# Performance work log

Measured on AMD Instinct MI355X. Metric: run time of the kernel, lower is better.

Reference implementation:

```python
import jax, jax.numpy as jnp
import numpy as np

D_MODEL = 768
N_HEADS = 12
D_K = D_MODEL // N_HEADS
NEG = -1e9


def setup_inputs() -> dict:
    key = jax.random.key(0)
    ks = jax.random.split(key, 10)
    B, S = 2, 2048
    x = jax.random.normal(ks[0], (B, S, D_MODEL), dtype=jnp.float32)
    # causal mask, broadcastable over batch and heads
    mask = jnp.tril(jnp.ones((S, S), dtype=jnp.int32))[None, None]
    scale = 1.0 / np.sqrt(D_MODEL)
    def lin(k):
        return jax.random.normal(k, (D_MODEL, D_MODEL), dtype=jnp.float32) * scale
    return {
        "x": x, "mask": mask,
        "wq": lin(ks[1]), "bq": jnp.zeros((D_MODEL,), jnp.float32),
        "wk": lin(ks[2]), "bk": jnp.zeros((D_MODEL,), jnp.float32),
        "wv": lin(ks[3]), "bv": jnp.zeros((D_MODEL,), jnp.float32),
        "wo": lin(ks[4]), "bo": jnp.zeros((D_MODEL,), jnp.float32),
    }


def reference(x, mask, wq, bq, wk, bk, wv, bv, wo, bo):
    B, S, _ = x.shape
    def split_heads(t):  # [B,S,D] -> [B,H,S,dk]
        return t.reshape(B, S, N_HEADS, D_K).transpose(0, 2, 1, 3)
    q = split_heads(x @ wq + bq)
    k = split_heads(x @ wk + bk)
    v = split_heads(x @ wv + bv)
    scores = jnp.einsum("bhqd,bhkd->bhqk", q, k) / jnp.sqrt(jnp.float32(D_K))
    scores = jnp.where(mask == 0, NEG, scores)
    attn = jax.nn.softmax(scores, axis=-1)
    # dropout is identity in eval mode
    ctx = jnp.einsum("bhqk,bhkd->bhqd", attn, v)
    ctx = ctx.transpose(0, 2, 1, 3).reshape(B, S, D_MODEL)
    return ctx @ wo + bo
```

## Files before the change

### kernel.cpp

```cpp
#include <hip/hip_runtime.h>
#include <hip/hip_bf16.h>
#include <stdint.h>

#define DM   768
#define NH   12
#define DKH  64
#define BB   2
#define SS   2048
#define MT   (BB*SS)
#define NQKV (3*DM)

typedef __attribute__((ext_vector_type(8))) short short8;
typedef __attribute__((ext_vector_type(4))) float f32x4;

__device__ __forceinline__ unsigned short f2bf(float f) {
    union { float f; unsigned u; } v; v.f = f;
    unsigned r = v.u + 0x7fffu + ((v.u >> 16) & 1u);
    return (unsigned short)(r >> 16);
}

__device__ __forceinline__ void gload_lds16(const unsigned short* g, unsigned short* l) {
    __builtin_amdgcn_global_load_lds((const __attribute__((address_space(1))) void*)g,
                                     (__attribute__((address_space(3))) void*)l, 16, 0, 0);
}

__launch_bounds__(256)
__global__ void k_conv(const float* __restrict__ x, unsigned short* __restrict__ xb,
                       const float* __restrict__ wq, const float* __restrict__ wk,
                       const float* __restrict__ wv, const float* __restrict__ wo,
                       unsigned short* __restrict__ wT) {
    __shared__ float tile[32][33];
    const int t = threadIdx.x;
    if (blockIdx.x < 3072) {
        int i = blockIdx.x * 256 + t;
        const float4 v = ((const float4*)x)[i];
        ushort4 o;
        o.x = f2bf(v.x); o.y = f2bf(v.y); o.z = f2bf(v.z); o.w = f2bf(v.w);
        ((ushort4*)xb)[i] = o;
    } else {
        const int cid = blockIdx.x - 3072;
        const int sel = cid / 576;
        const int rem = cid - sel * 576;
        const int kb = rem / 24, nb = rem - (rem / 24) * 24;
        const float* w = (sel == 0) ? wq : (sel == 1) ? wk : (sel == 2) ? wv : wo;
        const int k0 = kb * 32, n0 = nb * 32;
        const int tx = t & 31, ty = t >> 5;
        #pragma unroll
        for (int j = 0; j < 4; j++)
            tile[ty + 8*j][tx] = w[(size_t)(k0 + ty + 8*j) * DM + n0 + tx];
        __syncthreads();
        #pragma unroll
        for (int j = 0; j < 4; j++)
            wT[(size_t)(sel*DM + n0 + ty + 8*j) * DM + k0 + tx] = f2bf(tile[tx][ty + 8*j]);
    }
}

__launch_bounds__(256)
__global__ void k_gemm_qkv(const unsigned short* __restrict__ xb,
                           const unsigned short* __restrict__ wT,
                           const float* __restrict__ bq, const float* __restrict__ bk,
                           const float* __restrict__ bv,
                           unsigned short* __restrict__ Qb,
                           unsigned short* __restrict__ Kb,
                           unsigned short* __restrict__ Vt) {
    __shared__ __align__(16) unsigned short As[128][32];
    __shared__ __align__(16) unsigned short Bs[128][32];
    const int t = threadIdx.x;
    const int m0 = blockIdx.x * 128;
    const int n0 = blockIdx.y * 128;
    const int wid = t >> 6, lane = t & 63, q4 = lane >> 4, l16 = lane & 15;
    const int wm = (wid >> 1) * 64, wn = (wid & 1) * 64;

    const int srow = wid * 32 + (lane >> 2);
    const int koff = (lane & 3) * 8;
    const unsigned short* AgL = xb + (size_t)(m0 + srow) * DM + koff;
    const unsigned short* AgH = AgL + (size_t)16 * DM;
    const unsigned short* BgL = wT + (size_t)(n0 + srow) * DM + koff;
    const unsigned short* BgH = BgL + (size_t)16 * DM;
    unsigned short* ldsA1 = &As[wid*32][0];
    unsigned short* ldsA2 = &As[wid*32 + 16][0];
    unsigned short* ldsB1 = &Bs[wid*32][0];
    unsigned short* ldsB2 = &Bs[wid*32 + 16][0];

    f32x4 acc[4][4];
    for (int i = 0; i < 4; i++) for (int j = 0; j < 4; j++)
        acc[i][j] = (f32x4){0.f, 0.f, 0.f, 0.f};

    for (int kt = 0; kt < DM; kt += 32) {
        gload_lds16(AgL + kt, ldsA1);
        gload_lds16(AgH + kt, ldsA2);
        gload_lds16(BgL + kt, ldsB1);
        gload_lds16(BgH + kt, ldsB2);
        __syncthreads();
        short8 af[4], bf[4];
        for (int i = 0; i < 4; i++) af[i] = *(const short8*)&As[wm + i*16 + l16][q4*8];
        for (int i = 0; i < 4; i++) bf[i] = *(const short8*)&Bs[wn + i*16 + l16][q4*8];
        for (int mi = 0; mi < 4; mi++)
            for (int ni = 0; ni < 4; ni++)
                acc[mi][ni] = __builtin_amdgcn_mfma_f32_16x16x32_bf16(af[mi], bf[ni], acc[mi][ni], 0, 0, 0);
        __syncthreads();
    }

    const int sel = n0 / DM;
    const float* bias = (sel == 0) ? bq : (sel == 1) ? bk : bv;
    for (int ni = 0; ni < 4; ni++) {
        const int col = n0 + wn + ni*16 + l16;
        const int c = col - sel * DM;
        const float bsv = bias[c];
        const int h = c >> 6, d = c & 63;
        for (int mi = 0; mi < 4; mi++) {
            for (int r = 0; r < 4; r++) {
                const int row = m0 + wm + mi*16 + q4*4 + r;
                const int b = row >> 11, s = row & 2047;
                const int bh = b * NH + h;
                float v = acc[mi][ni][r] + bsv;
                if (sel == 0) {
                    Qb[(bh*SS + s)*DKH + d] = f2bf(v * 0.125f);
                } else if (sel == 1) {
                    Kb[(bh*SS + s)*DKH + d] = f2bf(v);
                } else {
                    Vt[(bh*DKH + d)*SS + s] = f2bf(v);
                }
            }
        }
    }
}

__launch_bounds__(256, 3)
__global__ void k_attn(const unsigned short* __restrict__ Qb,
                       const unsigned short* __restrict__ Kb,
                       const unsigned short* __restrict__ Vt,
                       unsigned short* __restrict__ ctx) {
    __shared__ __align__(16) unsigned short Ks[2][64*64];
    __shared__ __align__(16) unsigned short Vs[2][64*64];
    __shared__ __align__(16) unsigned short P2[4][32*64];
    const int t = threadIdx.x;
    const int wid = t >> 6, lane = t & 63, q4 = lane >> 4, l16 = lane & 15;

    const int lin = blockIdx.x;
    int g;
    if (lin < 128)      g = 128 + lin;
    else if (lin < 256) g = lin - 128;
    else                g = 639 - lin;
    const int bh  = g % 24;
    const int qsb = 15 - g / 24;
    const int KT  = 2*qsb + 1;
    const int b = bh / NH, h = bh - b * NH;
    const int qw = qsb*128 + wid*32;
    const int ktw = (qw + 31) >> 6;

    const unsigned short* Qp = Qb + (size_t)bh * SS * DKH;
    const unsigned short* Kp = Kb + (size_t)bh * SS * DKH;
    const unsigned short* Vp = Vt + (size_t)bh * DKH * SS;

    const int sr  = t >> 3;
    const int sc8 = (t & 7) * 8;
    const int scs = sc8 ^ ((sr & 7) * 8);
    const int swz = (l16 & 7) * 8;

    short8 qf[2][2];
    #pragma unroll
    for (int c = 0; c < 2; c++)
        #pragma unroll
        for (int kc = 0; kc < 2; kc++)
            qf[c][kc] = *(const short8*)(Qp + (size_t)(qw + c*16 + l16)*DKH + kc*32 + q4*8);

    f32x4 accO[2][4];
    #pragma unroll
    for (int c = 0; c < 2; c++)
        #pragma unroll
        for (int j = 0; j < 4; j++) accO[c][j] = (f32x4){0.f, 0.f, 0.f, 0.f};
    float lacc[2] = {0.f, 0.f};

    {
        *(uint4*)&Ks[0][ sr      *64 + scs] = *(const uint4*)(Kp + (size_t) sr      *DKH + sc8);
        *(uint4*)&Ks[0][(sr+32)*64 + scs]   = *(const uint4*)(Kp + (size_t)(sr+32)  *DKH + sc8);
        *(uint4*)&Vs[0][ sr      *64 + scs] = *(const uint4*)(Vp + (size_t) sr      *SS  + sc8);
        *(uint4*)&Vs[0][(sr+32)*64 + scs]   = *(const uint4*)(Vp + (size_t)(sr+32)  *SS  + sc8);
    }
    __syncthreads();

    for (int kt = 0; kt <= KT; kt++) {
        const int cb = kt & 1, nb = cb ^ 1;
        const bool hasN = (kt < KT);
        uint4 nk0, nk1, nv0, nv1;
        if (hasN) {
            const int kn = (kt + 1) * 64;
            nk0 = *(const uint4*)(Kp + (size_t)(kn + sr)      * DKH + sc8);
            nk1 = *(const uint4*)(Kp + (size_t)(kn + sr + 32) * DKH + sc8);
            nv0 = *(const uint4*)(Vp + (size_t)(sr)      * SS + kn + sc8);
            nv1 = *(const uint4*)(Vp + (size_t)(sr + 32) * SS + kn + sc8);
        }
        if (kt <= ktw) {
            f32x4 St[2][4];
            #pragma unroll
            for (int c = 0; c < 2; c++)
                #pragma unroll
                for (int ni = 0; ni < 4; ni++) St[c][ni] = (f32x4){0.f, 0.f, 0.f, 0.f};
            __builtin_amdgcn_s_setprio(1);
            #pragma unroll
            for (int ni = 0; ni < 4; ni++) {
                const int rbase = (ni*16 + l16) * 64;
                short8 kf0 = *(const short8*)&Ks[cb][rbase + ((     q4*8) ^ swz)];
                short8 kf1 = *(const short8*)&Ks[cb][rbase + ((32 + q4*8) ^ swz)];
                St[0][ni] = __builtin_amdgcn_mfma_f32_16x16x32_bf16(kf0, qf[0][0], St[0][ni], 0, 0, 0);
                St[0][ni] = __builtin_amdgcn_mfma_f32_16x16x32_bf16(kf1, qf[0][1], St[0][ni], 0, 0, 0);
                St[1][ni] = __builtin_amdgcn_mfma_f32_16x16x32_bf16(kf0, qf[1][0], St[1][ni], 0, 0, 0);
                St[1][ni] = __builtin_amdgcn_mfma_f32_16x16x32_bf16(kf1, qf[1][1], St[1][ni], 0, 0, 0);
            }
            __builtin_amdgcn_s_setprio(0);
            if (kt < ktw) {
                #pragma unroll
                for (int c = 0; c < 2; c++) {
                    const int prow = (c*16 + l16) * 64;
                    #pragma unroll
                    for (int ni = 0; ni < 4; ni++) {
                        float p0 = __expf(St[c][ni][0]), p1 = __expf(St[c][ni][1]);
                        float p2 = __expf(St[c][ni][2]), p3 = __expf(St[c][ni][3]);
                        lacc[c] += (p0 + p1) + (p2 + p3);
                        union { __hip_bfloat162 v; unsigned u; } u01, u23;
                        u01.v = __float22bfloat162_rn(make_float2(p0, p1));
                        u23.v = __float22bfloat162_rn(make_float2(p2, p3));
                        uint2 pk; pk.x = u01.u; pk.y = u23.u;
                        *(uint2*)&P2[wid][prow + ((ni*16 + q4*4) ^ swz)] = pk;
                    }
                }
            } else {
                const int kb0 = kt * 64;
                #pragma unroll
                for (int c = 0; c < 2; c++) {
                    const int qrow = qw + c*16 + l16;
                    const int prow = (c*16 + l16) * 64;
                    #pragma unroll
                    for (int ni = 0; ni < 4; ni++) {
                        const int key0 = kb0 + ni*16 + q4*4;
                        float p[4];
                        #pragma unroll
                        for (int r = 0; r < 4; r++) {
                            p[r] = (key0 + r > qrow) ? 0.f : __expf(St[c][ni][r]);
                            lacc[c] += p[r];
                        }
                        union { __hip_bfloat162 v; unsigned u; } u01, u23;
                        u01.v = __float22bfloat162_rn(make_float2(p[0], p[1]));
                        u23.v = __float22bfloat162_rn(make_float2(p[2], p[3]));
                        uint2 pk; pk.x = u01.u; pk.y = u23.u;
                        *(uint2*)&P2[wid][prow + ((ni*16 + q4*4) ^ swz)] = pk;
                    }
                }
            }
            asm volatile("s_waitcnt lgkmcnt(0)" ::: "memory");
            short8 pf[2][2];
            #pragma unroll
            for (int c = 0; c < 2; c++)
                #pragma unroll
                for (int kc = 0; kc < 2; kc++)
                    pf[c][kc] = *(const short8*)&P2[wid][(c*16 + l16)*64 + ((kc*32 + q4*8) ^ swz)];
            __builtin_amdgcn_s_setprio(1);
            #pragma unroll
            for (int ndi = 0; ndi < 4; ndi++) {
                const int rbase = (ndi*16 + l16) * 64;
                short8 vf0 = *(const short8*)&Vs[cb][rbase + ((     q4*8) ^ swz)];
                short8 vf1 = *(const short8*)&Vs[cb][rbase + ((32 + q4*8) ^ swz)];
                accO[0][ndi] = __builtin_amdgcn_mfma_f32_16x16x32_bf16(vf0, pf[0][0], accO[0][ndi], 0, 0, 0);
                accO[0][ndi] = __builtin_amdgcn_mfma_f32_16x16x32_bf16(vf1, pf[0][1], accO[0][ndi], 0, 0, 0);
                accO[1][ndi] = __builtin_amdgcn_mfma_f32_16x16x32_bf16(vf0, pf[1][0], accO[1][ndi], 0, 0, 0);
                accO[1][ndi] = __builtin_amdgcn_mfma_f32_16x16x32_bf16(vf1, pf[1][1], accO[1][ndi], 0, 0, 0);
            }
            __builtin_amdgcn_s_setprio(0);
        }
        if (hasN) {
            *(uint4*)&Ks[nb][ sr     *64 + scs] = nk0;
            *(uint4*)&Ks[nb][(sr+32)*64 + scs]  = nk1;
            *(uint4*)&Vs[nb][ sr     *64 + scs] = nv0;
            *(uint4*)&Vs[nb][(sr+32)*64 + scs]  = nv1;
        }
        __syncthreads();
    }

    #pragma unroll
    for (int c = 0; c < 2; c++) {
        float l = lacc[c];
        l += __shfl_xor(l, 16);
        l += __shfl_xor(l, 32);
        const float inv = 1.0f / l;
        const size_t row = (size_t)(b*SS + qw + c*16 + l16);
        #pragma unroll
        for (int ndi = 0; ndi < 4; ndi++) {
            ushort4 o;
            o.x = f2bf(accO[c][ndi][0] * inv);
            o.y = f2bf(accO[c][ndi][1] * inv);
            o.z = f2bf(accO[c][ndi][2] * inv);
            o.w = f2bf(accO[c][ndi][3] * inv);
            *(ushort4*)&ctx[row*DM + h*64 + ndi*16 + q4*4] = o;
        }
    }
}

__launch_bounds__(256)
__global__ void k_gemm_proj(const unsigned short* __restrict__ ctx,
                            const unsigned short* __restrict__ woT,
                            const float* __restrict__ bo,
                            float* __restrict__ out) {
    __shared__ __align__(16) unsigned short As[128][32];
    __shared__ __align__(16) unsigned short Bs[64][32];
    const int t = threadIdx.x;
    const int m0 = blockIdx.x * 128;
    const int n0 = blockIdx.y * 64;
    const int wid = t >> 6, lane = t & 63, q4 = lane >> 4, l16 = lane & 15;
    const int wm = (wid >> 1) * 64, wn = (wid & 1) * 32;

    const int srowA = wid * 32 + (lane >> 2);
    const int srowB = wid * 16 + (lane >> 2);
    const int koff = (lane & 3) * 8;
    const unsigned short* AgL = ctx + (size_t)(m0 + srowA) * DM + koff;
    const unsigned short* AgH = AgL + (size_t)16 * DM;
    const unsigned short* BgL = woT + (size_t)(n0 + srowB) * DM + koff;
    unsigned short* ldsA1 = &As[wid*32][0];
    unsigned short* ldsA2 = &As[wid*32 + 16][0];
    unsigned short* ldsB1 = &Bs[wid*16][0];

    f32x4 acc[4][2];
    for (int i = 0; i < 4; i++) for (int j = 0; j < 2; j++)
        acc[i][j] = (f32x4){0.f, 0.f, 0.f, 0.f};

    for (int kt = 0; kt < DM; kt += 32) {
        gload_lds16(AgL + kt, ldsA1);
        gload_lds16(AgH + kt, ldsA2);
        gload_lds16(BgL + kt, ldsB1);
        __syncthreads();
        short8 af[4], bf[2];
        for (int i = 0; i < 4; i++) af[i] = *(const short8*)&As[wm + i*16 + l16][q4*8];
        for (int i = 0; i < 2; i++) bf[i] = *(const short8*)&Bs[wn + i*16 + l16][q4*8];
        for (int mi = 0; mi < 4; mi++)
            for (int ni = 0; ni < 2; ni++)
                acc[mi][ni] = __builtin_amdgcn_mfma_f32_16x16x32_bf16(af[mi], bf[ni], acc[mi][ni], 0, 0, 0);
        __syncthreads();
    }

    for (int ni = 0; ni < 2; ni++) {
        const int col = n0 + wn + ni*16 + l16;
        const float bsv = bo[col];
        for (int mi = 0; mi < 4; mi++) {
            for (int r = 0; r < 4; r++) {
                const int row = m0 + wm + mi*16 + q4*4 + r;
                out[(size_t)row * DM + col] = acc[mi][ni][r] + bsv;
            }
        }
    }
}

extern "C" void kernel_launch(void* const* d_in, const int* in_sizes, int n_in,
                              void* d_out, int out_size, void* d_ws, size_t ws_size,
                              hipStream_t stream) {
    const float* x  = (const float*)d_in[0];
    const float* wq = (const float*)d_in[2];
    const float* bq = (const float*)d_in[3];
    const float* wk = (const float*)d_in[4];
    const float* bk = (const float*)d_in[5];
    const float* wv = (const float*)d_in[6];
    const float* bv = (const float*)d_in[7];
    const float* wo = (const float*)d_in[8];
    const float* bo = (const float*)d_in[9];
    float* out = (float*)d_out;

    unsigned short* xb  = (unsigned short*)d_ws;
    unsigned short* wT  = xb + (size_t)MT * DM;
    unsigned short* Qb  = wT + (size_t)4 * DM * DM;
    unsigned short* Kb  = Qb + (size_t)BB * NH * SS * DKH;
    unsigned short* Vt  = Kb + (size_t)BB * NH * SS * DKH;
    unsigned short* ctx = Vt + (size_t)BB * NH * SS * DKH;

    k_conv<<<3072 + 2304, 256, 0, stream>>>(x, xb, wq, wk, wv, wo, wT);
    dim3 g1(MT / 128, NQKV / 128);
    k_gemm_qkv<<<g1, 256, 0, stream>>>(xb, wT, bq, bk, bv, Qb, Kb, Vt);
    k_attn<<<dim3(384), 256, 0, stream>>>(Qb, Kb, Vt, ctx);
    dim3 g3(MT / 128, DM / 64);
    k_gemm_proj<<<g3, 256, 0, stream>>>(ctx, wT + (size_t)3 * DM * DM, bo, out);
}
```

Measured before the change: 185.0 us.

## Split attention into 64-row query blocks with split-KV for long rows

The attention kernel moves from 128-row query blocks to 64-row blocks (16 rows per wave). A static work table splits the key range of the longest query blocks into two chunks, giving 1152 roughly balanced blocks instead of 384. Partial unnormalized outputs and row sums for the split blocks go to a float workspace, and a new combine kernel merges them. This targets load imbalance and low occupancy in causal attention, and raises the occupancy hint to 4. The cost is an extra launch, fp32 partial traffic, and less K/V reuse per loaded tile.

```diff
diff --git a/kernel.cpp b/kernel.cpp
--- a/kernel.cpp
+++ b/kernel.cpp
@@ -126,28 +126,38 @@
     }
 }
 
-__launch_bounds__(256, 3)
+__device__ const int UNITS[48] = {
+  (15<<16)|(0<<8)|16, (31<<16)|(0<<8)|16, (31<<16)|(16<<8)|32, (30<<16)|(0<<8)|16,
+  (14<<16)|(0<<8)|15, (29<<16)|(0<<8)|15, (29<<16)|(15<<8)|30, (28<<16)|(0<<8)|15, (30<<16)|(16<<8)|31,
+  (13<<16)|(0<<8)|14, (27<<16)|(0<<8)|14, (27<<16)|(14<<8)|28, (26<<16)|(0<<8)|14, (28<<16)|(15<<8)|29,
+  (12<<16)|(0<<8)|13, (25<<16)|(0<<8)|13, (25<<16)|(13<<8)|26, (24<<16)|(0<<8)|13, (26<<16)|(14<<8)|27,
+  (11<<16)|(0<<8)|12, (23<<16)|(0<<8)|12, (23<<16)|(12<<8)|24, (22<<16)|(0<<8)|12, (24<<16)|(13<<8)|25,
+  (10<<16)|(0<<8)|11, (21<<16)|(0<<8)|11, (21<<16)|(11<<8)|22, (20<<16)|(0<<8)|11, (22<<16)|(12<<8)|23,
+  ( 9<<16)|(0<<8)|10, (19<<16)|(0<<8)|10, (19<<16)|(10<<8)|20, (18<<16)|(0<<8)|10, (20<<16)|(11<<8)|21,
+  ( 8<<16)|(0<<8)| 9, (17<<16)|(0<<8)| 9, (17<<16)|( 9<<8)|18, (16<<16)|(0<<8)| 9, (18<<16)|(10<<8)|19,
+  ( 7<<16)|(0<<8)| 8, (16<<16)|( 9<<8)|17,
+  ( 6<<16)|(0<<8)| 7, ( 5<<16)|(0<<8)| 6, ( 4<<16)|(0<<8)| 5, ( 3<<16)|(0<<8)| 4,
+  ( 2<<16)|(0<<8)| 3, ( 1<<16)|(0<<8)| 2, ( 0<<16)|(0<<8)| 1,
+};
+
+__launch_bounds__(256, 4)
 __global__ void k_attn(const unsigned short* __restrict__ Qb,
                        const unsigned short* __restrict__ Kb,
                        const unsigned short* __restrict__ Vt,
-                       unsigned short* __restrict__ ctx) {
+                       unsigned short* __restrict__ ctx,
+                       float* __restrict__ Opart, float* __restrict__ lpart) {
     __shared__ __align__(16) unsigned short Ks[2][64*64];
     __shared__ __align__(16) unsigned short Vs[2][64*64];
-    __shared__ __align__(16) unsigned short P2[4][32*64];
+    __shared__ __align__(16) unsigned short P2[4][16*64];
     const int t = threadIdx.x;
     const int wid = t >> 6, lane = t & 63, q4 = lane >> 4, l16 = lane & 15;
 
     const int lin = blockIdx.x;
-    int g;
-    if (lin < 128)      g = 128 + lin;
-    else if (lin < 256) g = lin - 128;
-    else                g = 639 - lin;
-    const int bh  = g % 24;
-    const int qsb = 15 - g / 24;
-    const int KT  = 2*qsb + 1;
+    const int bh = lin % 24;
+    const int info = UNITS[lin / 24];
+    const int qblk = info >> 16, t0 = (info >> 8) & 0xff, t1 = info & 0xff;
     const int b = bh / NH, h = bh - b * NH;
-    const int qw = qsb*128 + wid*32;
-    const int ktw = (qw + 31) >> 6;
+    const int qw = qblk * 64 + wid * 16;
 
     const unsigned short* Qp = Qb + (size_t)bh * SS * DKH;
     const unsigned short* Kp = Kb + (size_t)bh * SS * DKH;
@@ -158,31 +168,27 @@
     const int scs = sc8 ^ ((sr & 7) * 8);
     const int swz = (l16 & 7) * 8;
 
-    short8 qf[2][2];
+    short8 qf[2];
+    qf[0] = *(const short8*)(Qp + (size_t)(qw + l16)*DKH +      q4*8);
+    qf[1] = *(const short8*)(Qp + (size_t)(qw + l16)*DKH + 32 + q4*8);
+
+    f32x4 accO[4];
     #pragma unroll
-    for (int c = 0; c < 2; c++)
-        #pragma unroll
-        for (int kc = 0; kc < 2; kc++)
-            qf[c][kc] = *(const short8*)(Qp + (size_t)(qw + c*16 + l16)*DKH + kc*32 + q4*8);
-
-    f32x4 accO[2][4];
-    #pragma unroll
-    for (int c = 0; c < 2; c++)
-        #pragma unroll
-        for (int j = 0; j < 4; j++) accO[c][j] = (f32x4){0.f, 0.f, 0.f, 0.f};
-    float lacc[2] = {0.f, 0.f};
+    for (int j = 0; j < 4; j++) accO[j] = (f32x4){0.f, 0.f, 0.f, 0.f};
+    float lacc = 0.f;
 
     {
-        *(uint4*)&Ks[0][ sr      *64 + scs] = *(const uint4*)(Kp + (size_t) sr      *DKH + sc8);
-        *(uint4*)&Ks[0][(sr+32)*64 + scs]   = *(const uint4*)(Kp + (size_t)(sr+32)  *DKH + sc8);
-        *(uint4*)&Vs[0][ sr      *64 + scs] = *(const uint4*)(Vp + (size_t) sr      *SS  + sc8);
-        *(uint4*)&Vs[0][(sr+32)*64 + scs]   = *(const uint4*)(Vp + (size_t)(sr+32)  *SS  + sc8);
+        const int kb0 = t0 * 64;
+        *(uint4*)&Ks[0][ sr    *64 + scs] = *(const uint4*)(Kp + (size_t)(kb0 + sr)     *DKH + sc8);
+        *(uint4*)&Ks[0][(sr+32)*64 + scs] = *(const uint4*)(Kp + (size_t)(kb0 + sr + 32)*DKH + sc8);
+        *(uint4*)&Vs[0][ sr    *64 + scs] = *(const uint4*)(Vp + (size_t) sr     *SS + kb0 + sc8);
+        *(uint4*)&Vs[0][(sr+32)*64 + scs] = *(const uint4*)(Vp + (size_t)(sr+32) *SS + kb0 + sc8);
     }
     __syncthreads();
 
-    for (int kt = 0; kt <= KT; kt++) {
-        const int cb = kt & 1, nb = cb ^ 1;
-        const bool hasN = (kt < KT);
+    for (int kt = t0; kt < t1; kt++) {
+        const int cb = (kt - t0) & 1, nb = cb ^ 1;
+        const bool hasN = (kt + 1 < t1);
         uint4 nk0, nk1, nv0, nv1;
         if (hasN) {
             const int kn = (kt + 1) * 64;
@@ -191,108 +197,124 @@
             nv0 = *(const uint4*)(Vp + (size_t)(sr)      * SS + kn + sc8);
             nv1 = *(const uint4*)(Vp + (size_t)(sr + 32) * SS + kn + sc8);
         }
-        if (kt <= ktw) {
-            f32x4 St[2][4];
-            #pragma unroll
-            for (int c = 0; c < 2; c++)
-                #pragma unroll
-                for (int ni = 0; ni < 4; ni++) St[c][ni] = (f32x4){0.f, 0.f, 0.f, 0.f};
-            __builtin_amdgcn_s_setprio(1);
+        f32x4 St[4];
+        #pragma unroll
+        for (int ni = 0; ni < 4; ni++) St[ni] = (f32x4){0.f, 0.f, 0.f, 0.f};
+        __builtin_amdgcn_s_setprio(1);
+        #pragma unroll
+        for (int ni = 0; ni < 4; ni++) {
+            const int rbase = (ni*16 + l16) * 64;
+            short8 kf0 = *(const short8*)&Ks[cb][rbase + ((     q4*8) ^ swz)];
+            short8 kf1 = *(const short8*)&Ks[cb][rbase + ((32 + q4*8) ^ swz)];
+            St[ni] = __builtin_amdgcn_mfma_f32_16x16x32_bf16(kf0, qf[0], St[ni], 0, 0, 0);
+            St[ni] = __builtin_amdgcn_mfma_f32_16x16x32_bf16(kf1, qf[1], St[ni], 0, 0, 0);
+        }
+        __builtin_amdgcn_s_setprio(0);
+        if (kt < qblk) {
             #pragma unroll
             for (int ni = 0; ni < 4; ni++) {
-                const int rbase = (ni*16 + l16) * 64;
-                short8 kf0 = *(const short8*)&Ks[cb][rbase + ((     q4*8) ^ swz)];
-                short8 kf1 = *(const short8*)&Ks[cb][rbase + ((32 + q4*8) ^ swz)];
-                St[0][ni] = __builtin_amdgcn_mfma_f32_16x16x32_bf16(kf0, qf[0][0], St[0][ni], 0, 0, 0);
-                St[0][ni] = __builtin_amdgcn_mfma_f32_16x16x32_bf16(kf1, qf[0][1], St[0][ni], 0, 0, 0);
-                St[1][ni] = __builtin_amdgcn_mfma_f32_16x16x32_bf16(kf0, qf[1][0], St[1][ni], 0, 0, 0);
-                St[1][ni] = __builtin_amdgcn_mfma_f32_16x16x32_bf16(kf1, qf[1][1], St[1][ni], 0, 0, 0);
+                float p0 = __expf(St[ni][0]), p1 = __expf(St[ni][1]);
+                float p2 = __expf(St[ni][2]), p3 = __expf(St[ni][3]);
+                lacc += (p0 + p1) + (p2 + p3);
+                union { __hip_bfloat162 v; unsigned u; } u01, u23;
+                u01.v = __float22bfloat162_rn(make_float2(p0, p1));
+                u23.v = __float22bfloat162_rn(make_float2(p2, p3));
+                uint2 pk; pk.x = u01.u; pk.y = u23.u;
+                *(uint2*)&P2[wid][l16*64 + ((ni*16 + q4*4) ^ swz)] = pk;
             }
-            __builtin_amdgcn_s_setprio(0);
-            if (kt < ktw) {
+        } else {
+            const int qrow = qw + l16;
+            #pragma unroll
+            for (int ni = 0; ni < 4; ni++) {
+                const int key0 = kt*64 + ni*16 + q4*4;
+                float p[4];
                 #pragma unroll
-                for (int c = 0; c < 2; c++) {
-                    const int prow = (c*16 + l16) * 64;
-                    #pragma unroll
-                    for (int ni = 0; ni < 4; ni++) {
-                        float p0 = __expf(St[c][ni][0]), p1 = __expf(St[c][ni][1]);
-                        float p2 = __expf(St[c][ni][2]), p3 = __expf(St[c][ni][3]);
-                        lacc[c] += (p0 + p1) + (p2 + p3);
-                        union { __hip_bfloat162 v; unsigned u; } u01, u23;
-                        u01.v = __float22bfloat162_rn(make_float2(p0, p1));
-                        u23.v = __float22bfloat162_rn(make_float2(p2, p3));
-                        uint2 pk; pk.x = u01.u; pk.y = u23.u;
-                        *(uint2*)&P2[wid][prow + ((ni*16 + q4*4) ^ swz)] = pk;
-                    }
+                for (int r = 0; r < 4; r++) {
+                    p[r] = (key0 + r > qrow) ? 0.f : __expf(St[ni][r]);
+                    lacc += p[r];
                 }
-            } else {
-                const int kb0 = kt * 64;
-                #pragma unroll
-                for (int c = 0; c < 2; c++) {
-                    const int qrow = qw + c*16 + l16;
-                    const int prow = (c*16 + l16) * 64;
-                    #pragma unroll
-                    for (int ni = 0; ni < 4; ni++) {
-                        const int key0 = kb0 + ni*16 + q4*4;
-                        float p[4];
-                        #pragma unroll
-                        for (int r = 0; r < 4; r++) {
-                            p[r] = (key0 + r > qrow) ? 0.f : __expf(St[c][ni][r]);
-                            lacc[c] += p[r];
-                        }
-                        union { __hip_bfloat162 v; unsigned u; } u01, u23;
-                        u01.v = __float22bfloat162_rn(make_float2(p[0], p[1]));
-                        u23.v = __float22bfloat162_rn(make_float2(p[2], p[3]));
-                        uint2 pk; pk.x = u01.u; pk.y = u23.u;
-                        *(uint2*)&P2[wid][prow + ((ni*16 + q4*4) ^ swz)] = pk;
-                    }
-                }
+                union { __hip_bfloat162 v; unsigned u; } u01, u23;
+                u01.v = __float22bfloat162_rn(make_float2(p[0], p[1]));
+                u23.v = __float22bfloat162_rn(make_float2(p[2], p[3]));
+                uint2 pk; pk.x = u01.u; pk.y = u23.u;
+                *(uint2*)&P2[wid][l16*64 + ((ni*16 + q4*4) ^ swz)] = pk;
             }
-            asm volatile("s_waitcnt lgkmcnt(0)" ::: "memory");
-            short8 pf[2][2];
-            #pragma unroll
-            for (int c = 0; c < 2; c++)
-                #pragma unroll
-                for (int kc = 0; kc < 2; kc++)
-                    pf[c][kc] = *(const short8*)&P2[wid][(c*16 + l16)*64 + ((kc*32 + q4*8) ^ swz)];
-            __builtin_amdgcn_s_setprio(1);
-            #pragma unroll
-            for (int ndi = 0; ndi < 4; ndi++) {
-                const int rbase = (ndi*16 + l16) * 64;
-                short8 vf0 = *(const short8*)&Vs[cb][rbase + ((     q4*8) ^ swz)];
-                short8 vf1 = *(const short8*)&Vs[cb][rbase + ((32 + q4*8) ^ swz)];
-                accO[0][ndi] = __builtin_amdgcn_mfma_f32_16x16x32_bf16(vf0, pf[0][0], accO[0][ndi], 0, 0, 0);
-                accO[0][ndi] = __builtin_amdgcn_mfma_f32_16x16x32_bf16(vf1, pf[0][1], accO[0][ndi], 0, 0, 0);
-                accO[1][ndi] = __builtin_amdgcn_mfma_f32_16x16x32_bf16(vf0, pf[1][0], accO[1][ndi], 0, 0, 0);
-                accO[1][ndi] = __builtin_amdgcn_mfma_f32_16x16x32_bf16(vf1, pf[1][1], accO[1][ndi], 0, 0, 0);
-            }
-            __builtin_amdgcn_s_setprio(0);
-        }
+        }
+        asm volatile("s_waitcnt lgkmcnt(0)" ::: "memory");
+        short8 pf[2];
+        pf[0] = *(const short8*)&P2[wid][l16*64 + ((     q4*8) ^ swz)];
+        pf[1] = *(const short8*)&P2[wid][l16*64 + ((32 + q4*8) ^ swz)];
+        __builtin_amdgcn_s_setprio(1);
+        #pragma unroll
+        for (int ndi = 0; ndi < 4; ndi++) {
+            const int rbase = (ndi*16 + l16) * 64;
+            short8 vf0 = *(const short8*)&Vs[cb][rbase + ((     q4*8) ^ swz)];
+            short8 vf1 = *(const short8*)&Vs[cb][rbase + ((32 + q4*8) ^ swz)];
+            accO[ndi] = __builtin_amdgcn_mfma_f32_16x16x32_bf16(vf0, pf[0], accO[ndi], 0, 0, 0);
+            accO[ndi] = __builtin_amdgcn_mfma_f32_16x16x32_bf16(vf1, pf[1], accO[ndi], 0, 0, 0);
+        }
+        __builtin_amdgcn_s_setprio(0);
         if (hasN) {
-            *(uint4*)&Ks[nb][ sr     *64 + scs] = nk0;
-            *(uint4*)&Ks[nb][(sr+32)*64 + scs]  = nk1;
-            *(uint4*)&Vs[nb][ sr     *64 + scs] = nv0;
-            *(uint4*)&Vs[nb][(sr+32)*64 + scs]  = nv1;
-        }
-        __syncthreads();
-    }
-
-    #pragma unroll
-    for (int c = 0; c < 2; c++) {
-        float l = lacc[c];
-        l += __shfl_xor(l, 16);
-        l += __shfl_xor(l, 32);
+            *(uint4*)&Ks[nb][ sr    *64 + scs] = nk0;
+            *(uint4*)&Ks[nb][(sr+32)*64 + scs] = nk1;
+            *(uint4*)&Vs[nb][ sr    *64 + scs] = nv0;
+            *(uint4*)&Vs[nb][(sr+32)*64 + scs] = nv1;
+        }
+        __syncthreads();
+    }
+
+    float l = lacc;
+    l += __shfl_xor(l, 16);
+    l += __shfl_xor(l, 32);
+
+    if (qblk < 16) {
         const float inv = 1.0f / l;
-        const size_t row = (size_t)(b*SS + qw + c*16 + l16);
+        const size_t row = (size_t)(b*SS + qw + l16);
         #pragma unroll
         for (int ndi = 0; ndi < 4; ndi++) {
             ushort4 o;
-            o.x = f2bf(accO[c][ndi][0] * inv);
-            o.y = f2bf(accO[c][ndi][1] * inv);
-            o.z = f2bf(accO[c][ndi][2] * inv);
-            o.w = f2bf(accO[c][ndi][3] * inv);
+            o.x = f2bf(accO[ndi][0] * inv);
+            o.y = f2bf(accO[ndi][1] * inv);
+            o.z = f2bf(accO[ndi][2] * inv);
+            o.w = f2bf(accO[ndi][3] * inv);
             *(ushort4*)&ctx[row*DM + h*64 + ndi*16 + q4*4] = o;
         }
+    } else {
+        const int pair  = bh * 16 + (qblk - 16);
+        const int chunk = (t0 != 0);
+        const int qloc  = wid * 16 + l16;
+        float* Op = Opart + ((size_t)pair * 2 + chunk) * 4096;
+        #pragma unroll
+        for (int ndi = 0; ndi < 4; ndi++)
+            *(f32x4*)&Op[qloc*64 + ndi*16 + q4*4] = accO[ndi];
+        if (q4 == 0) lpart[pair*128 + chunk*64 + qloc] = l;
+    }
+}
+
+__launch_bounds__(256)
+__global__ void k_combine(const float* __restrict__ Opart,
+                          const float* __restrict__ lpart,
+                          unsigned short* __restrict__ ctx) {
+    const int pair = blockIdx.x;
+    const int bh = pair >> 4, qblk = 16 + (pair & 15);
+    const int b = bh / NH, h = bh - b * NH;
+    const int t = threadIdx.x;
+    const int q = t >> 2, dg = (t & 3) * 16;
+    const float* P0 = Opart + (size_t)pair * 2 * 4096;
+    const float* P1 = P0 + 4096;
+    const float* L0 = lpart + pair * 128;
+    const float inv = 1.0f / (L0[q] + L0[64 + q]);
+    const size_t row = (size_t)(b*SS + qblk*64 + q);
+    #pragma unroll
+    for (int i = 0; i < 4; i++) {
+        f32x4 a = *(const f32x4*)&P0[q*64 + dg + i*4];
+        f32x4 c = *(const f32x4*)&P1[q*64 + dg + i*4];
+        ushort4 o;
+        o.x = f2bf((a[0] + c[0]) * inv);
+        o.y = f2bf((a[1] + c[1]) * inv);
+        o.z = f2bf((a[2] + c[2]) * inv);
+        o.w = f2bf((a[3] + c[3]) * inv);
+        *(ushort4*)&ctx[row*DM + h*64 + dg + i*4] = o;
     }
 }
 
@@ -369,11 +391,14 @@
     unsigned short* Kb  = Qb + (size_t)BB * NH * SS * DKH;
     unsigned short* Vt  = Kb + (size_t)BB * NH * SS * DKH;
     unsigned short* ctx = Vt + (size_t)BB * NH * SS * DKH;
+    float* Opart = (float*)(ctx + (size_t)MT * DM);
+    float* lpart = Opart + (size_t)768 * 4096;
 
     k_conv<<<3072 + 2304, 256, 0, stream>>>(x, xb, wq, wk, wv, wo, wT);
     dim3 g1(MT / 128, NQKV / 128);
     k_gemm_qkv<<<g1, 256, 0, stream>>>(xb, wT, bq, bk, bv, Qb, Kb, Vt);
-    k_attn<<<dim3(384), 256, 0, stream>>>(Qb, Kb, Vt, ctx);
+    k_attn<<<dim3(1152), 256, 0, stream>>>(Qb, Kb, Vt, ctx, Opart, lpart);
+    k_combine<<<dim3(384), 256, 0, stream>>>(Opart, lpart, ctx);
     dim3 g3(MT / 128, DM / 64);
     k_gemm_proj<<<g3, 256, 0, stream>>>(ctx, wT + (size_t)3 * DM * DM, bo, out);
 }
```

Result: faster. 168.7 us (-8.8%).

## Split long causal attention query blocks across KV chunks with combine kernel

Applied to the files above, without the earlier changes.

The attention kernel now splits each query block's key range into up to four KV chunks (split-K / flash-decoding style), raising the grid from 384 to 960 blocks via a static work-unit table ordered longest-first. Partial unnormalized outputs and row sums go to a float workspace, and a new combine kernel sums them and normalizes into ctx. This targets load imbalance and low occupancy from causal triangular work on 256 CUs. It costs an extra kernel launch plus partial-result traffic, and depends on the absence of per-row max rescaling so that partials can simply be summed.

```diff
diff --git a/kernel.cpp b/kernel.cpp
--- a/kernel.cpp
+++ b/kernel.cpp
@@ -126,11 +126,36 @@
     }
 }
 
+#define U(q,c,a,b2) (((q)<<16)|((c)<<12)|((a)<<6)|(b2))
+__device__ const int UNITS[40] = {
+  U(15,0,0,8),  U(15,1,8,16),  U(15,2,16,24), U(15,3,24,32),
+  U(14,0,0,8),  U(14,1,8,16),
+  U(11,0,0,8),  U(11,1,8,16),  U(11,2,16,24),
+  U(10,0,0,8),
+  U(7,0,0,8),   U(7,1,8,16),
+  U(3,0,0,8),
+  U(14,2,16,23), U(14,3,23,30),
+  U(13,0,0,7),  U(13,1,7,14),  U(13,2,14,21), U(13,3,21,28),
+  U(12,0,0,7),  U(12,1,7,14),
+  U(10,1,8,15), U(10,2,15,22),
+  U(9,0,0,7),   U(9,1,7,14),
+  U(6,0,0,7),   U(6,1,7,14),
+  U(12,2,14,20), U(12,3,20,26),
+  U(9,2,14,20),
+  U(8,0,0,6),   U(8,1,6,12),   U(8,2,12,18),
+  U(5,0,0,6),   U(5,1,6,12),
+  U(2,0,0,6),
+  U(4,0,0,5),   U(4,1,5,10),
+  U(1,0,0,4),
+  U(0,0,0,2),
+};
+
 __launch_bounds__(256, 3)
 __global__ void k_attn(const unsigned short* __restrict__ Qb,
                        const unsigned short* __restrict__ Kb,
                        const unsigned short* __restrict__ Vt,
-                       unsigned short* __restrict__ ctx) {
+                       unsigned short* __restrict__ ctx,
+                       float* __restrict__ Opart, float* __restrict__ lpart) {
     __shared__ __align__(16) unsigned short Ks[2][64*64];
     __shared__ __align__(16) unsigned short Vs[2][64*64];
     __shared__ __align__(16) unsigned short P2[4][32*64];
@@ -138,13 +163,11 @@
     const int wid = t >> 6, lane = t & 63, q4 = lane >> 4, l16 = lane & 15;
 
     const int lin = blockIdx.x;
-    int g;
-    if (lin < 128)      g = 128 + lin;
-    else if (lin < 256) g = lin - 128;
-    else                g = 639 - lin;
-    const int bh  = g % 24;
-    const int qsb = 15 - g / 24;
-    const int KT  = 2*qsb + 1;
+    const int bh = lin % 24;
+    const int info = UNITS[lin / 24];
+    const int qsb = info >> 16, ci = (info >> 12) & 0xf;
+    const int t0 = (info >> 6) & 0x3f, t1 = info & 0x3f;
+    const int nch = (2*qsb + 9) >> 3;
     const int b = bh / NH, h = bh - b * NH;
     const int qw = qsb*128 + wid*32;
     const int ktw = (qw + 31) >> 6;
@@ -173,16 +196,17 @@
     float lacc[2] = {0.f, 0.f};
 
     {
-        *(uint4*)&Ks[0][ sr      *64 + scs] = *(const uint4*)(Kp + (size_t) sr      *DKH + sc8);
-        *(uint4*)&Ks[0][(sr+32)*64 + scs]   = *(const uint4*)(Kp + (size_t)(sr+32)  *DKH + sc8);
-        *(uint4*)&Vs[0][ sr      *64 + scs] = *(const uint4*)(Vp + (size_t) sr      *SS  + sc8);
-        *(uint4*)&Vs[0][(sr+32)*64 + scs]   = *(const uint4*)(Vp + (size_t)(sr+32)  *SS  + sc8);
+        const int kb0 = t0 * 64;
+        *(uint4*)&Ks[0][ sr    *64 + scs] = *(const uint4*)(Kp + (size_t)(kb0 + sr)     *DKH + sc8);
+        *(uint4*)&Ks[0][(sr+32)*64 + scs] = *(const uint4*)(Kp + (size_t)(kb0 + sr + 32)*DKH + sc8);
+        *(uint4*)&Vs[0][ sr    *64 + scs] = *(const uint4*)(Vp + (size_t) sr     *SS + kb0 + sc8);
+        *(uint4*)&Vs[0][(sr+32)*64 + scs] = *(const uint4*)(Vp + (size_t)(sr+32) *SS + kb0 + sc8);
     }
     __syncthreads();
 
-    for (int kt = 0; kt <= KT; kt++) {
-        const int cb = kt & 1, nb = cb ^ 1;
-        const bool hasN = (kt < KT);
+    for (int kt = t0; kt < t1; kt++) {
+        const int cb = (kt - t0) & 1, nb = cb ^ 1;
+        const bool hasN = (kt + 1 < t1);
         uint4 nk0, nk1, nv0, nv1;
         if (hasN) {
             const int kn = (kt + 1) * 64;
@@ -269,29 +293,80 @@
             __builtin_amdgcn_s_setprio(0);
         }
         if (hasN) {
-            *(uint4*)&Ks[nb][ sr     *64 + scs] = nk0;
-            *(uint4*)&Ks[nb][(sr+32)*64 + scs]  = nk1;
-            *(uint4*)&Vs[nb][ sr     *64 + scs] = nv0;
-            *(uint4*)&Vs[nb][(sr+32)*64 + scs]  = nv1;
-        }
-        __syncthreads();
-    }
-
+            *(uint4*)&Ks[nb][ sr    *64 + scs] = nk0;
+            *(uint4*)&Ks[nb][(sr+32)*64 + scs] = nk1;
+            *(uint4*)&Vs[nb][ sr    *64 + scs] = nv0;
+            *(uint4*)&Vs[nb][(sr+32)*64 + scs] = nv1;
+        }
+        __syncthreads();
+    }
+
+    if (nch == 1) {
+        #pragma unroll
+        for (int c = 0; c < 2; c++) {
+            float l = lacc[c];
+            l += __shfl_xor(l, 16);
+            l += __shfl_xor(l, 32);
+            const float inv = 1.0f / l;
+            const size_t row = (size_t)(b*SS + qw + c*16 + l16);
+            #pragma unroll
+            for (int ndi = 0; ndi < 4; ndi++) {
+                ushort4 o;
+                o.x = f2bf(accO[c][ndi][0] * inv);
+                o.y = f2bf(accO[c][ndi][1] * inv);
+                o.z = f2bf(accO[c][ndi][2] * inv);
+                o.w = f2bf(accO[c][ndi][3] * inv);
+                *(ushort4*)&ctx[row*DM + h*64 + ndi*16 + q4*4] = o;
+            }
+        }
+    } else {
+        const int slot = (bh*16 + qsb)*4 + ci;
+        float* Op = Opart + (size_t)slot * 8192;
+        #pragma unroll
+        for (int c = 0; c < 2; c++) {
+            float l = lacc[c];
+            l += __shfl_xor(l, 16);
+            l += __shfl_xor(l, 32);
+            const int qloc = wid*32 + c*16 + l16;
+            #pragma unroll
+            for (int ndi = 0; ndi < 4; ndi++)
+                *(f32x4*)&Op[qloc*64 + ndi*16 + q4*4] = accO[c][ndi];
+            if (q4 == 0) lpart[slot*128 + qloc] = l;
+        }
+    }
+}
+
+__launch_bounds__(256)
+__global__ void k_combine(const float* __restrict__ Opart,
+                          const float* __restrict__ lpart,
+                          unsigned short* __restrict__ ctx) {
+    const int pair = blockIdx.x;
+    const int bh = pair / 12, qsb = 4 + pair % 12;
+    const int nch = (2*qsb + 9) >> 3;
+    const int b = bh / NH, h = bh - b * NH;
+    const int s0 = (bh*16 + qsb)*4;
+    const int t = threadIdx.x;
     #pragma unroll
-    for (int c = 0; c < 2; c++) {
-        float l = lacc[c];
-        l += __shfl_xor(l, 16);
-        l += __shfl_xor(l, 32);
-        const float inv = 1.0f / l;
-        const size_t row = (size_t)(b*SS + qw + c*16 + l16);
-        #pragma unroll
-        for (int ndi = 0; ndi < 4; ndi++) {
+    for (int it = 0; it < 2; it++) {
+        const int q = (t >> 2) + it*64;
+        const int dg = (t & 3) * 16;
+        float lsum = 0.f;
+        for (int ci = 0; ci < nch; ci++) lsum += lpart[(s0 + ci)*128 + q];
+        const float inv = 1.0f / lsum;
+        const size_t row = (size_t)(b*SS + qsb*128 + q);
+        #pragma unroll
+        for (int i = 0; i < 4; i++) {
+            f32x4 a = (f32x4){0.f, 0.f, 0.f, 0.f};
+            for (int ci = 0; ci < nch; ci++) {
+                f32x4 c = *(const f32x4*)&Opart[(size_t)(s0 + ci)*8192 + q*64 + dg + i*4];
+                a[0] += c[0]; a[1] += c[1]; a[2] += c[2]; a[3] += c[3];
+            }
             ushort4 o;
-            o.x = f2bf(accO[c][ndi][0] * inv);
-            o.y = f2bf(accO[c][ndi][1] * inv);
-            o.z = f2bf(accO[c][ndi][2] * inv);
-            o.w = f2bf(accO[c][ndi][3] * inv);
-            *(ushort4*)&ctx[row*DM + h*64 + ndi*16 + q4*4] = o;
+            o.x = f2bf(a[0] * inv);
+            o.y = f2bf(a[1] * inv);
+            o.z = f2bf(a[2] * inv);
+            o.w = f2bf(a[3] * inv);
+            *(ushort4*)&ctx[row*DM + h*64 + dg + i*4] = o;
         }
     }
 }
@@ -369,11 +444,14 @@
     unsigned short* Kb  = Qb + (size_t)BB * NH * SS * DKH;
     unsigned short* Vt  = Kb + (size_t)BB * NH * SS * DKH;
     unsigned short* ctx = Vt + (size_t)BB * NH * SS * DKH;
+    float* Opart = (float*)(ctx + (size_t)MT * DM);
+    float* lpart = Opart + (size_t)24 * 16 * 4 * 8192;
 
     k_conv<<<3072 + 2304, 256, 0, stream>>>(x, xb, wq, wk, wv, wo, wT);
     dim3 g1(MT / 128, NQKV / 128);
     k_gemm_qkv<<<g1, 256, 0, stream>>>(xb, wT, bq, bk, bv, Qb, Kb, Vt);
-    k_attn<<<dim3(384), 256, 0, stream>>>(Qb, Kb, Vt, ctx);
+    k_attn<<<dim3(960), 256, 0, stream>>>(Qb, Kb, Vt, ctx, Opart, lpart);
+    k_combine<<<dim3(288), 256, 0, stream>>>(Opart, lpart, ctx);
     dim3 g3(MT / 128, DM / 64);
     k_gemm_proj<<<g3, 256, 0, stream>>>(ctx, wT + (size_t)3 * DM * DM, bo, out);
 }
```

New measurement: 181.5 us. Within noise of the previous version (-1.9%).
